# Performance work log

Measured on AMD Instinct MI355X. Metric: run time of the kernel, lower is better.

Reference implementation:

```python
import jax, jax.numpy as jnp
import numpy as np

N_NODES = 10000
N_EDGES = 320000
NODE_F = 64
EDGE_F = 32
H = 256
L = 6
HEADS = 8
OUT = H // HEADS
N_GRAPHS = 16
NEG_SLOPE = 0.2  # PyG GATConv leaky_relu slope


def setup_inputs() -> dict:
    key = jax.random.key(0)
    ks = jax.random.split(key, 32)
    s = 0.05
    f32 = jnp.float32
    inp = {}
    inp["x"] = jax.random.normal(ks[0], (N_NODES, NODE_F), f32)
    inp["edge_index"] = jax.random.randint(ks[1], (2, N_EDGES), 0, N_NODES)
    inp["edge_attr"] = jax.random.normal(ks[2], (N_EDGES, EDGE_F), f32)
    inp["batch"] = jnp.sort(jax.random.randint(ks[3], (N_NODES,), 0, N_GRAPHS))
    # embeddings
    inp["node_w"] = jax.random.normal(ks[4], (H, NODE_F), f32) * s
    inp["node_b"] = jnp.zeros((H,), f32)
    inp["edge_emb_w"] = jax.random.normal(ks[5], (H, EDGE_F), f32) * s
    inp["edge_emb_b"] = jnp.zeros((H,), f32)
    # stacked GATConv params (shared lin for src/dst since in_channels is int)
    inp["lin_w"] = jax.random.normal(ks[6], (L, H, H), f32) * s
    inp["att_src"] = jax.random.normal(ks[7], (L, HEADS, OUT), f32) * s
    inp["att_dst"] = jax.random.normal(ks[8], (L, HEADS, OUT), f32) * s
    inp["att_edge"] = jax.random.normal(ks[9], (L, HEADS, OUT), f32) * s
    inp["lin_edge_w"] = jax.random.normal(ks[10], (L, H, H), f32) * s
    inp["conv_b"] = jnp.zeros((L, H), f32)
    inp["ln_g"] = jnp.ones((L, H), f32)
    inp["ln_b"] = jnp.zeros((L, H), f32)
    # MLP heads: Linear(2H->H), Linear(H->H/2), Linear(H/2->3)
    inp["pw1"] = jax.random.normal(ks[11], (H, 2 * H), f32) * s
    inp["pb1"] = jnp.zeros((H,), f32)
    inp["pw2"] = jax.random.normal(ks[12], (H // 2, H), f32) * s
    inp["pb2"] = jnp.zeros((H // 2,), f32)
    inp["pw3"] = jax.random.normal(ks[13], (3, H // 2), f32) * s
    inp["pb3"] = jnp.zeros((3,), f32)
    inp["mw1"] = jax.random.normal(ks[14], (H, 2 * H), f32) * s
    inp["mb1"] = jnp.zeros((H,), f32)
    inp["mw2"] = jax.random.normal(ks[15], (H // 2, H), f32) * s
    inp["mb2"] = jnp.zeros((H // 2,), f32)
    inp["mw3"] = jax.random.normal(ks[16], (3, H // 2), f32) * s
    inp["mb3"] = jnp.zeros((3,), f32)
    return inp


def _ln(x, g, b):
    mu = jnp.mean(x, -1, keepdims=True)
    var = jnp.mean(jnp.square(x - mu), -1, keepdims=True)
    return g * (x - mu) * jax.lax.rsqrt(var + 1e-5) + b


def _mlp(z, w1, b1, w2, b2, w3, b3):
    h = jax.nn.gelu(z @ w1.T + b1, approximate=False)
    h = jax.nn.gelu(h @ w2.T + b2, approximate=False)
    return jax.nn.sigmoid(h @ w3.T + b3)


def _gnn_forward(x, edge_attr, src, dst, batch,
                 node_w, node_b, edge_emb_w, edge_emb_b,
                 lin_w, att_src, att_dst, att_edge, lin_edge_w, conv_b,
                 ln_g, ln_b,
                 pw1, pb1, pw2, pb2, pw3, pb3,
                 mw1, mb1, mw2, mb2, mw3, mb3):
    h = x @ node_w.T + node_b                       # [N, H]
    ea = edge_attr @ edge_emb_w.T + edge_emb_b      # [E, H]
    # PyG add_self_loops(fill_value='mean'): loop attr = mean of incoming edge attrs
    cnt = jax.ops.segment_sum(jnp.ones((N_EDGES,), h.dtype), dst, N_NODES)
    loop_attr = jax.ops.segment_sum(ea, dst, N_NODES) / jnp.maximum(cnt, 1.0)[:, None]
    ea_full = jnp.concatenate([ea, loop_attr], 0)   # [E+N, H]
    loops = jnp.arange(N_NODES, dtype=src.dtype)
    src_f = jnp.concatenate([src, loops])
    dst_f = jnp.concatenate([dst, loops])
    for i in range(L):
        x_in = h
        xw = (h @ lin_w[i].T).reshape(N_NODES, HEADS, OUT)
        eap = (ea_full @ lin_edge_w[i].T).reshape(-1, HEADS, OUT)
        a_src = jnp.sum(xw * att_src[i], -1)        # [N, heads]
        a_dst = jnp.sum(xw * att_dst[i], -1)
        alpha = a_src[src_f] + a_dst[dst_f] + jnp.sum(eap * att_edge[i], -1)  # [E+N, heads]
        alpha = jnp.where(alpha > 0, alpha, NEG_SLOPE * alpha)
        amax = jax.ops.segment_max(alpha, dst_f, N_NODES)
        e = jnp.exp(alpha - amax[dst_f])
        denom = jax.ops.segment_sum(e, dst_f, N_NODES)
        w = e / (denom[dst_f] + 1e-16)
        msg = xw[src_f] * w[:, :, None]             # [E+N, heads, out]
        hi = jax.ops.segment_sum(msg, dst_f, N_NODES).reshape(N_NODES, H) + conv_b[i]
        hi = jax.nn.gelu(_ln(hi, ln_g[i], ln_b[i]), approximate=False)
        h = hi + x_in if i > 0 else hi
    sums = jax.ops.segment_sum(h, batch, N_GRAPHS)  # [G, H]
    ncnt = jax.ops.segment_sum(jnp.ones((N_NODES,), h.dtype), batch, N_GRAPHS)
    mean = sums / jnp.maximum(ncnt, 1.0)[:, None]
    xg = jnp.concatenate([mean, sums], 1)           # [G, 2H]
    params = _mlp(xg, pw1, pb1, pw2, pb2, pw3, pb3)
    metrics = _mlp(xg, mw1, mb1, mw2, mb2, mw3, mb3)
    return params, metrics


def reference(x, edge_index, edge_attr, batch,
              node_w, node_b, edge_emb_w, edge_emb_b,
              lin_w, att_src, att_dst, att_edge, lin_edge_w, conv_b,
              ln_g, ln_b,
              pw1, pb1, pw2, pb2, pw3, pb3,
              mw1, mb1, mw2, mb2, mw3, mb3):
    return _gnn_forward(x, edge_attr, edge_index[0], edge_index[1], batch,
                        node_w, node_b, edge_emb_w, edge_emb_b,
                        lin_w, att_src, att_dst, att_edge, lin_edge_w, conv_b,
                        ln_g, ln_b,
                        pw1, pb1, pw2, pb2, pw3, pb3,
                        mw1, mb1, mw2, mb2, mw3, mb3)
```

## Files before the change

kernel.cpp:

```cpp
#include <hip/hip_runtime.h>
#include <math.h>

#define NN 10000
#define NE 320000
#define NODE_F 64
#define EDGE_F 32
#define HDIM 256
#define HEADS 8
#define LAYERS 6
#define NG 16
#define NPB 2
#define NOUT 48
#define LOG2E 1.4426950408889634f

typedef __attribute__((ext_vector_type(8))) short short8;
typedef __attribute__((ext_vector_type(4))) float float4v;
typedef __attribute__((ext_vector_type(2))) float floatx2;

__global__ void count_kernel(const int* __restrict__ dst, int* __restrict__ cnt) {
    int e = blockIdx.x * 256 + threadIdx.x;
    if (e < NE) atomicAdd(&cnt[dst[e]], 1);
}

__global__ void scan_kernel(const int* __restrict__ cnt, int* __restrict__ row_ptr,
                            int* __restrict__ pos) {
    __shared__ int wsum[16];
    __shared__ int woff[16];
    int t = threadIdx.x;
    int lane = t & 63, wid = t >> 6;
    const int chunk = 10;
    int lo = t * chunk;
    int loc[10];
    int s = 0;
    #pragma unroll
    for (int k = 0; k < 10; ++k) {
        int i = lo + k;
        int v = (i < NN) ? cnt[i] : 0;
        loc[k] = v;
        s += v;
    }
    int inc = s;
    #pragma unroll
    for (int off = 1; off < 64; off <<= 1) {
        int v = __shfl_up(inc, off, 64);
        if (lane >= off) inc += v;
    }
    if (lane == 63) wsum[wid] = inc;
    __syncthreads();
    if (t < 16) {
        int inc2 = wsum[t];
        #pragma unroll
        for (int off = 1; off < 16; off <<= 1) {
            int u = __shfl_up(inc2, off, 16);
            if (t >= off) inc2 += u;
        }
        woff[t] = inc2;
    }
    __syncthreads();
    int base = inc - s + (wid ? woff[wid - 1] : 0);
    #pragma unroll
    for (int k = 0; k < 10; ++k) {
        int i = lo + k;
        if (i < NN) {
            row_ptr[i] = base;
            pos[i] = base;
            base += loc[k];
        }
    }
    if (t == 1023) row_ptr[NN] = woff[15];
}

__global__ void scatter_kernel(const int* __restrict__ src, const int* __restrict__ dst,
                               int* __restrict__ pos, int2* __restrict__ csr_se) {
    int e = blockIdx.x * 256 + threadIdx.x;
    if (e >= NE) return;
    int d = dst[e];
    int idx = atomicAdd(&pos[d], 1);
    csr_se[idx] = make_int2(src[e], e);
}

__device__ __forceinline__ ushort f2bf(float f) {
    union { float f; unsigned u; } v; v.f = f;
    unsigned u = v.u;
    return (ushort)((u + 0x7fffu + ((u >> 16) & 1u)) >> 16);
}
__device__ __forceinline__ float bf2f(ushort b) {
    union { unsigned u; float f; } v; v.u = ((unsigned)b) << 16; return v.f;
}

__global__ __launch_bounds__(256) void prep_kernel(const float* __restrict__ att_edge,
                                                   const float* __restrict__ lin_edge_w,
                                                   const float* __restrict__ eew,
                                                   const float* __restrict__ eeb,
                                                   ushort* __restrict__ webbf,
                                                   float* __restrict__ bebuf) {
    int ih = blockIdx.x;
    int i = ih >> 3, h = ih & 7;
    __shared__ float vsh[HDIM];
    int t = threadIdx.x;
    float s = 0.f;
    const float* ae = att_edge + ih * 32;
    const float* lw = lin_edge_w + ((size_t)i * HDIM + h * 32) * HDIM + t;
    #pragma unroll
    for (int o = 0; o < 32; ++o) s += ae[o] * lw[(size_t)o * HDIM];
    vsh[t] = s;
    __syncthreads();
    if (t < EDGE_F) {
        float acc = 0.f;
        for (int k = 0; k < HDIM; ++k) acc += vsh[k] * eew[k * EDGE_F + t];
        webbf[ih * EDGE_F + t] = f2bf(acc * LOG2E);
    } else if (t == EDGE_F) {
        float acc = 0.f;
        for (int k = 0; k < HDIM; ++k) acc += vsh[k] * eeb[k];
        bebuf[ih] = acc * LOG2E;
    }
}

__global__ __launch_bounds__(64) void fold0_kernel(const float* __restrict__ lin_w,
                                                   const float* __restrict__ node_w,
                                                   const float* __restrict__ node_b,
                                                   ushort* __restrict__ w0p,
                                                   float* __restrict__ b0p) {
    int j = blockIdx.x, f = threadIdx.x;
    const float* wr = lin_w + (size_t)j * HDIM;
    float acc = 0.f, accb = 0.f;
    for (int k = 0; k < HDIM; ++k) acc += wr[k] * node_w[k * NODE_F + f];
    #pragma unroll
    for (int m = 0; m < 4; ++m) {
        int k = f + 64 * m;
        accb += wr[k] * node_b[k];
    }
    w0p[j * NODE_F + f] = f2bf(acc);
    #pragma unroll
    for (int off = 32; off >= 1; off >>= 1) accb += __shfl_xor(accb, off, 64);
    if (f == 0) b0p[j] = accb;
}

__global__ __launch_bounds__(256) void preE_kernel(const float* __restrict__ edge_attr,
                                                   const ushort* __restrict__ web,
                                                   const float* __restrict__ be,
                                                   ushort* __restrict__ preEb) {
    int wv = threadIdx.x >> 6, l = threadIdx.x & 63;
    int base = blockIdx.x * 64 + wv * 16;
    int m = l & 15, kq = (l >> 4) * 8;
    const float* ar = edge_attr + (size_t)(base + m) * EDGE_F + kq;
    float4 a0 = *(const float4*)(ar);
    float4 a1 = *(const float4*)(ar + 4);
    short8 afrag;
    afrag[0] = (short)f2bf(a0.x); afrag[1] = (short)f2bf(a0.y);
    afrag[2] = (short)f2bf(a0.z); afrag[3] = (short)f2bf(a0.w);
    afrag[4] = (short)f2bf(a1.x); afrag[5] = (short)f2bf(a1.y);
    afrag[6] = (short)f2bf(a1.z); afrag[7] = (short)f2bf(a1.w);
    float4v zero = {0.f, 0.f, 0.f, 0.f};
    float4v acc[3];
    #pragma unroll
    for (int ct = 0; ct < 3; ++ct) {
        short8 bfrag = *(const short8*)(web + (size_t)(ct * 16 + m) * EDGE_F + kq);
        acc[ct] = __builtin_amdgcn_mfma_f32_16x16x32_bf16(afrag, bfrag, zero, 0, 0, 0);
    }
    #pragma unroll
    for (int ct = 0; ct < 3; ++ct) {
        int oc = ct * 16 + m;
        int li = oc >> 3, hh = oc & 7;
        float bv = be[oc];
        #pragma unroll
        for (int r = 0; r < 4; ++r) {
            int row = (l >> 4) * 4 + r;
            preEb[(size_t)li * NE * 8 + (size_t)(base + row) * 8 + hh] = f2bf(acc[ct][r] + bv);
        }
    }
}

__global__ void tobf_all_kernel(const float* __restrict__ lin_w,
                                const float* __restrict__ x, ushort* __restrict__ wbhi,
                                ushort* __restrict__ xhi) {
    const int N1 = LAYERS * HDIM * HDIM;
    const int N2 = N1 + NN * NODE_F;
    int i = blockIdx.x * 256 + threadIdx.x;
    if (i < N1) wbhi[i] = f2bf(lin_w[i]);
    else if (i < N2) xhi[i - N1] = f2bf(x[i - N1]);
}

__global__ __launch_bounds__(128) void gemm_bf1(const ushort* __restrict__ Ah,
                                                const ushort* __restrict__ Bh,
                                                const float* __restrict__ bias,
                                                unsigned char* __restrict__ Cf8,
                                                const float* __restrict__ att_s,
                                                const float* __restrict__ att_d,
                                                float* __restrict__ a_src,
                                                float* __restrict__ a_dst,
                                                int N, int K) {
    __shared__ ushort sAh[64][40], sBh[64][40];
    int nb = blockIdx.y * 64, jb = blockIdx.x * 64;
    int t = threadIdx.x, w = t >> 6, l = t & 63;
    int srow = t >> 1, sq = (t & 1) * 16;
    int fr = l & 15, fq = (l >> 4) * 8;
    float4v acc[2][4] = {};
    for (int kt = 0; kt < K; kt += 32) {
        int gr = nb + srow;
        short8 a0 = {0,0,0,0,0,0,0,0}, a1 = {0,0,0,0,0,0,0,0};
        if (gr < N) {
            const short8* pa = (const short8*)(Ah + (size_t)gr * K + kt + sq);
            a0 = pa[0]; a1 = pa[1];
        }
        *(short8*)&sAh[srow][sq] = a0; *(short8*)&sAh[srow][sq + 8] = a1;
        const short8* pb = (const short8*)(Bh + (size_t)(jb + srow) * K + kt + sq);
        short8 b0 = pb[0], b1 = pb[1];
        *(short8*)&sBh[srow][sq] = b0; *(short8*)&sBh[srow][sq + 8] = b1;
        __syncthreads();
        short8 bh[4];
        #pragma unroll
        for (int nt = 0; nt < 4; ++nt)
            bh[nt] = *(const short8*)&sBh[nt * 16 + fr][fq];
        #pragma unroll
        for (int mt = 0; mt < 2; ++mt) {
            short8 ah = *(const short8*)&sAh[w * 32 + mt * 16 + fr][fq];
            #pragma unroll
            for (int nt = 0; nt < 4; ++nt)
                acc[mt][nt] = __builtin_amdgcn_mfma_f32_16x16x32_bf16(ah, bh[nt], acc[mt][nt], 0, 0, 0);
        }
        __syncthreads();
    }
    if (bias) {
        #pragma unroll
        for (int nt = 0; nt < 4; ++nt) {
            float bv = bias[jb + nt * 16 + fr];
            #pragma unroll
            for (int mt = 0; mt < 2; ++mt)
                #pragma unroll
                for (int r = 0; r < 4; ++r) acc[mt][nt][r] += bv;
        }
    }
    #pragma unroll
    for (int mt = 0; mt < 2; ++mt) {
        #pragma unroll
        for (int nt = 0; nt < 4; ++nt) {
            int col = jb + nt * 16 + fr;
            #pragma unroll
            for (int r = 0; r < 4; ++r) {
                int row = nb + w * 32 + mt * 16 + (l >> 4) * 4 + r;
                if (row < N) {
                    float v = acc[mt][nt][r];
                    int pk8 = __builtin_amdgcn_cvt_pk_fp8_f32(v, v, 0, false);
                    Cf8[(size_t)row * HDIM + col] = (unsigned char)(pk8 & 0xff);
                }
            }
        }
    }
    {
        int head0 = jb >> 5;
        float cs[4], cd[4];
        #pragma unroll
        for (int nt = 0; nt < 4; ++nt) {
            cs[nt] = att_s[jb + nt * 16 + fr] * LOG2E;
            cd[nt] = att_d[jb + nt * 16 + fr] * LOG2E;
        }
        #pragma unroll
        for (int mt = 0; mt < 2; ++mt) {
            #pragma unroll
            for (int r = 0; r < 4; ++r) {
                float s0 = acc[mt][0][r] * cs[0] + acc[mt][1][r] * cs[1];
                float s1 = acc[mt][2][r] * cs[2] + acc[mt][3][r] * cs[3];
                float d0 = acc[mt][0][r] * cd[0] + acc[mt][1][r] * cd[1];
                float d1 = acc[mt][2][r] * cd[2] + acc[mt][3][r] * cd[3];
                #pragma unroll
                for (int off = 8; off >= 1; off >>= 1) {
                    s0 += __shfl_xor(s0, off, 16);
                    s1 += __shfl_xor(s1, off, 16);
                    d0 += __shfl_xor(d0, off, 16);
                    d1 += __shfl_xor(d1, off, 16);
                }
                if (fr == 0) {
                    int row = nb + w * 32 + mt * 16 + (l >> 4) * 4 + r;
                    if (row < N) {
                        a_src[row * 8 + head0]     = s0;
                        a_src[row * 8 + head0 + 1] = s1;
                        a_dst[row * 8 + head0]     = d0;
                        a_dst[row * 8 + head0 + 1] = d1;
                    }
                }
            }
        }
    }
}

__device__ __forceinline__ float gelu_exact(float x) {
    return 0.5f * x * (1.f + erff(x * 0.70710678118654752f));
}

__global__ __launch_bounds__(64 * NPB) void node_kernel(const unsigned char* __restrict__ xwf8,
                                                  const ushort* __restrict__ pb,
                                                  const float* __restrict__ a_src,
                                                  const float* __restrict__ a_dst,
                                                  const int* __restrict__ row_ptr,
                                                  const int2* __restrict__ csr_se,
                                                  const ushort* __restrict__ hp,
                                                  ushort* __restrict__ hout,
                                                  const float* __restrict__ cb,
                                                  const float* __restrict__ lg,
                                                  const float* __restrict__ lb, int first) {
    int wv = threadIdx.x >> 6, l = threadIdx.x & 63;
    int n = blockIdx.x * NPB + wv;
    int start = row_ptr[n], end = row_ptr[n + 1];
    int hc = l >> 3;
    int hc8 = l & 56;
    int jj = l & 7;
    float adnh = a_dst[n * 8 + hc];
    const unsigned char* xb = xwf8 + 4 * l;

    float den = 0.f, acc[4] = {0.f, 0.f, 0.f, 0.f};
    float psum = 0.f;
    for (int idx = start; idx < end; idx += 8) {
        int myi = idx + jj;
        bool valid = myi < end;
        int2 se = valid ? csr_se[myi] : make_int2(n, 0);
        int snj[8];
        #pragma unroll
        for (int j = 0; j < 8; ++j) snj[j] = __shfl(se.x, hc8 + j, 64);
        unsigned g[8];
        #pragma unroll
        for (int j = 0; j < 8; ++j) g[j] = *(const unsigned*)(xb + (size_t)snj[j] * HDIM);
        float w_t = 0.f;
        if (valid) {
            float p_t = bf2f(pb[(size_t)se.y * 8 + hc]);
            float a_t = a_src[(size_t)se.x * 8 + hc] + adnh + p_t;
            w_t = exp2f(fminf(fmaxf(a_t, 0.2f * a_t), 57.7f));
            psum += p_t;
        }
        #pragma unroll
        for (int j = 0; j < 8; ++j) {
            float wj = __shfl(w_t, hc8 + j, 64);
            floatx2 lo = __builtin_amdgcn_cvt_pk_f32_fp8(g[j], false);
            floatx2 hi = __builtin_amdgcn_cvt_pk_f32_fp8(g[j], true);
            den += wj;
            acc[0] += wj * lo.x;
            acc[1] += wj * lo.y;
            acc[2] += wj * hi.x;
            acc[3] += wj * hi.y;
        }
    }
    #pragma unroll
    for (int off = 1; off < 8; off <<= 1) psum += __shfl_xor(psum, off, 64);
    int deg = end - start;
    float preLv = deg > 0 ? psum / (float)deg : 0.f;
    {
        float al = a_src[n * 8 + hc] + adnh + preLv;
        al = fminf(fmaxf(al, 0.2f * al), 57.7f);
        float wself = exp2f(al);
        den += wself;
        unsigned gs = *(const unsigned*)(xb + (size_t)n * HDIM);
        floatx2 lo = __builtin_amdgcn_cvt_pk_f32_fp8(gs, false);
        floatx2 hi = __builtin_amdgcn_cvt_pk_f32_fp8(gs, true);
        acc[0] += wself * lo.x;
        acc[1] += wself * lo.y;
        acc[2] += wself * hi.x;
        acc[3] += wself * hi.y;
    }
    float4 cb4 = *(const float4*)(cb + 4 * l);
    float invh = 1.f / (den + 1e-16f);
    acc[0] = acc[0] * invh + cb4.x;
    acc[1] = acc[1] * invh + cb4.y;
    acc[2] = acc[2] * invh + cb4.z;
    acc[3] = acc[3] * invh + cb4.w;

    float part = acc[0] + acc[1] + acc[2] + acc[3];
    #pragma unroll
    for (int off = 32; off >= 1; off >>= 1) part += __shfl_xor(part, off, 64);
    float mu = part * (1.f / 256.f);
    float p2 = 0.f;
    #pragma unroll
    for (int j = 0; j < 4; ++j) {
        float d = acc[j] - mu;
        p2 += d * d;
    }
    #pragma unroll
    for (int off = 32; off >= 1; off >>= 1) p2 += __shfl_xor(p2, off, 64);
    float rstd = rsqrtf(p2 * (1.f / 256.f) + 1e-5f);

    float4 lg4 = *(const float4*)(lg + 4 * l);
    float4 lb4 = *(const float4*)(lb + 4 * l);
    float o4[4];
    float lgv[4] = {lg4.x, lg4.y, lg4.z, lg4.w};
    float lbv[4] = {lb4.x, lb4.y, lb4.z, lb4.w};
    float hpv[4] = {0.f, 0.f, 0.f, 0.f};
    if (!first) {
        uint2 ph = *(const uint2*)(hp + (size_t)n * HDIM + 4 * l);
        hpv[0] = bf2f((ushort)(ph.x & 0xffff));
        hpv[1] = bf2f((ushort)(ph.x >> 16));
        hpv[2] = bf2f((ushort)(ph.y & 0xffff));
        hpv[3] = bf2f((ushort)(ph.y >> 16));
    }
    #pragma unroll
    for (int j = 0; j < 4; ++j) {
        float y = (acc[j] - mu) * rstd * lgv[j] + lbv[j];
        o4[j] = gelu_exact(y) + hpv[j];
    }
    uint2 po;
    po.x = (unsigned)f2bf(o4[0]) | ((unsigned)f2bf(o4[1]) << 16);
    po.y = (unsigned)f2bf(o4[2]) | ((unsigned)f2bf(o4[3]) << 16);
    *(uint2*)(hout + (size_t)n * HDIM + 4 * l) = po;
}

__global__ __launch_bounds__(256) void graph_sum_kernel(const ushort* __restrict__ h,
                                                        const int* __restrict__ batch,
                                                        float* __restrict__ sums) {
    int t = threadIdx.x;
    int n0 = blockIdx.x * 64;
    int n1 = min(NN, n0 + 64);
    float acc = 0.f;
    int cur = batch[n0];
    for (int n = n0; n < n1; ++n) {
        int b = batch[n];
        if (b != cur) {
            atomicAdd(&sums[cur * HDIM + t], acc);
            acc = 0.f;
            cur = b;
        }
        acc += bf2f(h[(size_t)n * HDIM + t]);
    }
    atomicAdd(&sums[cur * HDIM + t], acc);
}

__device__ __forceinline__ int lower_bound_dev(const int* a, int n, int v) {
    int lo = 0, hi = n;
    while (lo < hi) {
        int mid = (lo + hi) >> 1;
        if (a[mid] < v) lo = mid + 1; else hi = mid;
    }
    return lo;
}

__global__ __launch_bounds__(256) void mlp_kernel(const float* __restrict__ sums,
                                                  const int* __restrict__ batch,
                                                  const float* __restrict__ pw1,
                                                  const float* __restrict__ pb1,
                                                  const float* __restrict__ pw2,
                                                  const float* __restrict__ pb2,
                                                  const float* __restrict__ pw3,
                                                  const float* __restrict__ pb3,
                                                  const float* __restrict__ mw1,
                                                  const float* __restrict__ mb1,
                                                  const float* __restrict__ mw2,
                                                  const float* __restrict__ mb2,
                                                  const float* __restrict__ mw3,
                                                  const float* __restrict__ mb3,
                                                  float* __restrict__ out) {
    int g = blockIdx.x, which = blockIdx.y;
    const float* w1 = which ? mw1 : pw1; const float* b1 = which ? mb1 : pb1;
    const float* w2 = which ? mw2 : pw2; const float* b2 = which ? mb2 : pb2;
    const float* w3 = which ? mw3 : pw3; const float* b3 = which ? mb3 : pb3;
    __shared__ float xg[512];
    __shared__ float h1[256];
    __shared__ float h2[128];
    __shared__ float cinv_s;
    int t = threadIdx.x;
    if (t == 0) {
        int s0 = lower_bound_dev(batch, NN, g), s1 = lower_bound_dev(batch, NN, g + 1);
        cinv_s = 1.f / fmaxf((float)(s1 - s0), 1.f);
    }
    __syncthreads();
    float sv = sums[g * HDIM + t];
    xg[t] = sv * cinv_s;
    xg[256 + t] = sv;
    __syncthreads();
    {
        const float* wr = w1 + (size_t)t * 512;
        float acc = 0.f;
        #pragma unroll 8
        for (int k = 0; k < 512; k += 4) {
            float4 wv = *(const float4*)(wr + k);
            acc += wv.x * xg[k] + wv.y * xg[k + 1] + wv.z * xg[k + 2] + wv.w * xg[k + 3];
        }
        h1[t] = gelu_exact(acc + b1[t]);
    }
    __syncthreads();
    {
        int row = t >> 1, hf = t & 1;
        const float* wr = w2 + (size_t)row * 256 + hf * 128;
        const float* hx = h1 + hf * 128;
        float acc = 0.f;
        #pragma unroll 8
        for (int k = 0; k < 128; k += 4) {
            float4 wv = *(const float4*)(wr + k);
            acc += wv.x * hx[k] + wv.y * hx[k + 1] + wv.z * hx[k + 2] + wv.w * hx[k + 3];
        }
        acc += __shfl_xor(acc, 1, 64);
        if (hf == 0) h2[row] = gelu_exact(acc + b2[row]);
    }
    __syncthreads();
    if (t < 64) {
        float v0 = h2[t], v1 = h2[64 + t];
        #pragma unroll
        for (int o = 0; o < 3; ++o) {
            float p = w3[o * 128 + t] * v0 + w3[o * 128 + 64 + t] * v1;
            #pragma unroll
            for (int off = 32; off >= 1; off >>= 1) p += __shfl_xor(p, off, 64);
            if (t == 0) out[which * (NG * 3) + g * 3 + o] = 1.f / (1.f + expf(-(p + b3[o])));
        }
    }
}

extern "C" void kernel_launch(void* const* d_in, const int* in_sizes, int n_in, void* d_out,
                              int out_size, void* d_ws, size_t ws_size, hipStream_t stream) {
    const float* x         = (const float*)d_in[0];
    const int*   ei        = (const int*)d_in[1];
    const int*   src       = ei;
    const int*   dst       = ei + NE;
    const float* edge_attr = (const float*)d_in[2];
    const int*   batch     = (const int*)d_in[3];
    const float* node_w    = (const float*)d_in[4];
    const float* node_b    = (const float*)d_in[5];
    const float* eew       = (const float*)d_in[6];
    const float* eeb       = (const float*)d_in[7];
    const float* lin_w     = (const float*)d_in[8];
    const float* att_src   = (const float*)d_in[9];
    const float* att_dst   = (const float*)d_in[10];
    const float* att_edge  = (const float*)d_in[11];
    const float* lin_edge_w= (const float*)d_in[12];
    const float* conv_b    = (const float*)d_in[13];
    const float* ln_g      = (const float*)d_in[14];
    const float* ln_b      = (const float*)d_in[15];
    const float* pw1 = (const float*)d_in[16]; const float* pb1 = (const float*)d_in[17];
    const float* pw2 = (const float*)d_in[18]; const float* pb2 = (const float*)d_in[19];
    const float* pw3 = (const float*)d_in[20]; const float* pb3 = (const float*)d_in[21];
    const float* mw1 = (const float*)d_in[22]; const float* mb1 = (const float*)d_in[23];
    const float* mw2 = (const float*)d_in[24]; const float* mb2 = (const float*)d_in[25];
    const float* mw3 = (const float*)d_in[26]; const float* mb3 = (const float*)d_in[27];
    float* out = (float*)d_out;

    float* wsf = (float*)d_ws;
    float* a_src     = wsf; wsf += (size_t)NN * HEADS;
    float* a_dst     = wsf; wsf += (size_t)NN * HEADS;
    float* bebuf     = wsf; wsf += 64;
    float* b0p       = wsf; wsf += HDIM;
    ushort* ubuf = (ushort*)wsf;
    ushort* preEb = ubuf; ubuf += (size_t)NE * NOUT;
    ushort* webbf = ubuf; ubuf += (size_t)NOUT * EDGE_F;
    ushort* hb0  = ubuf; ubuf += (size_t)NN * HDIM;
    ushort* hb1  = ubuf; ubuf += (size_t)NN * HDIM;
    unsigned char* xwf8 = (unsigned char*)ubuf; ubuf += (size_t)NN * HDIM / 2;
    ushort* wbhi = ubuf; ubuf += (size_t)LAYERS * HDIM * HDIM;
    ushort* xhi  = ubuf; ubuf += (size_t)NN * NODE_F;
    ushort* w0p  = ubuf; ubuf += (size_t)HDIM * NODE_F;
    int* ibuf    = (int*)ubuf;
    int* cnt     = ibuf; ibuf += NN + 16;
    float* sums  = (float*)ibuf; ibuf += NG * HDIM;
    int* row_ptr = ibuf; ibuf += NN + 16;
    int* pos     = ibuf; ibuf += NN + 16;
    int2* csr_se = (int2*)ibuf; ibuf += 2 * NE;

    hipMemsetAsync(cnt, 0, (NN + 16 + NG * HDIM) * sizeof(int), stream);
    count_kernel<<<(NE + 255) / 256, 256, 0, stream>>>(dst, cnt);
    scan_kernel<<<1, 1024, 0, stream>>>(cnt, row_ptr, pos);
    scatter_kernel<<<(NE + 255) / 256, 256, 0, stream>>>(src, dst, pos, csr_se);

    prep_kernel<<<LAYERS * HEADS, 256, 0, stream>>>(att_edge, lin_edge_w, eew, eeb, webbf, bebuf);
    preE_kernel<<<NE / 64, 256, 0, stream>>>(edge_attr, webbf, bebuf, preEb);

    {
        const int total = LAYERS * HDIM * HDIM + NN * NODE_F;
        tobf_all_kernel<<<(total + 255) / 256, 256, 0, stream>>>(lin_w, x, wbhi, xhi);
    }
    fold0_kernel<<<HDIM, 64, 0, stream>>>(lin_w, node_w, node_b, w0p, b0p);

    ushort* hb[2] = {hb0, hb1};
    for (int i = 0; i < LAYERS; ++i) {
        dim3 grid(HDIM / 64, (NN + 63) / 64);
        const ushort* Ain = (i == 0) ? xhi : hb[(i - 1) & 1];
        const ushort* Bin = (i == 0) ? w0p : wbhi + (size_t)i * HDIM * HDIM;
        int Kin = (i == 0) ? NODE_F : HDIM;
        const float* bias = (i == 0) ? b0p : nullptr;
        gemm_bf1<<<grid, 128, 0, stream>>>(Ain, Bin, bias, xwf8,
                                           att_src + i * HEADS * 32, att_dst + i * HEADS * 32,
                                           a_src, a_dst, NN, Kin);
        node_kernel<<<NN / NPB, 64 * NPB, 0, stream>>>(
            xwf8, preEb + (size_t)i * NE * 8, a_src, a_dst,
            row_ptr, csr_se, (i == 0) ? nullptr : hb[(i - 1) & 1], hb[i & 1],
            conv_b + i * HDIM, ln_g + i * HDIM, ln_b + i * HDIM, i == 0 ? 1 : 0);
    }

    graph_sum_kernel<<<(NN + 63) / 64, 256, 0, stream>>>(hb[(LAYERS - 1) & 1], batch, sums);
    {
        dim3 gm(NG, 2);
        mlp_kernel<<<gm, 256, 0, stream>>>(sums, batch, pw1, pb1, pw2, pb2, pw3, pb3,
                                           mw1, mb1, mw2, mb2, mw3, mb3, out);
    }
}
```

Baseline: 477.3 us.

## Split node aggregation across two waves per node and fuse degree count into preE

The node kernel now assigns one node per 128-thread block. The two waves take alternating 8-edge chunks of the neighbor list and combine their partial sums through shared memory before the layernorm/GELU epilogue. This is meant to halve the serial gather latency per node and raise memory-level parallelism, at the cost of a sync, LDS traffic and duplicated epilogue math. The separate degree-counting kernel is also folded into preE_kernel, which removes one launch.

```diff
diff --git a/kernel.cpp b/kernel.cpp
--- a/kernel.cpp
+++ b/kernel.cpp
@@ -9,18 +9,12 @@
 #define HEADS 8
 #define LAYERS 6
 #define NG 16
-#define NPB 2
 #define NOUT 48
 #define LOG2E 1.4426950408889634f
 
 typedef __attribute__((ext_vector_type(8))) short short8;
 typedef __attribute__((ext_vector_type(4))) float float4v;
 typedef __attribute__((ext_vector_type(2))) float floatx2;
-
-__global__ void count_kernel(const int* __restrict__ dst, int* __restrict__ cnt) {
-    int e = blockIdx.x * 256 + threadIdx.x;
-    if (e < NE) atomicAdd(&cnt[dst[e]], 1);
-}
 
 __global__ void scan_kernel(const int* __restrict__ cnt, int* __restrict__ row_ptr,
                             int* __restrict__ pos) {
@@ -139,8 +133,12 @@
 __global__ __launch_bounds__(256) void preE_kernel(const float* __restrict__ edge_attr,
                                                    const ushort* __restrict__ web,
                                                    const float* __restrict__ be,
-                                                   ushort* __restrict__ preEb) {
-    int wv = threadIdx.x >> 6, l = threadIdx.x & 63;
+                                                   ushort* __restrict__ preEb,
+                                                   const int* __restrict__ dst,
+                                                   int* __restrict__ cnt) {
+    int t = threadIdx.x;
+    if (t < 64) atomicAdd(&cnt[dst[blockIdx.x * 64 + t]], 1);
+    int wv = t >> 6, l = t & 63;
     int base = blockIdx.x * 64 + wv * 16;
     int m = l & 15, kq = (l >> 4) * 8;
     const float* ar = edge_attr + (size_t)(base + m) * EDGE_F + kq;
@@ -288,7 +286,7 @@
     return 0.5f * x * (1.f + erff(x * 0.70710678118654752f));
 }
 
-__global__ __launch_bounds__(64 * NPB) void node_kernel(const unsigned char* __restrict__ xwf8,
+__global__ __launch_bounds__(128) void node_kernel(const unsigned char* __restrict__ xwf8,
                                                   const ushort* __restrict__ pb,
                                                   const float* __restrict__ a_src,
                                                   const float* __restrict__ a_dst,
@@ -299,8 +297,10 @@
                                                   const float* __restrict__ cb,
                                                   const float* __restrict__ lg,
                                                   const float* __restrict__ lb, int first) {
-    int wv = threadIdx.x >> 6, l = threadIdx.x & 63;
-    int n = blockIdx.x * NPB + wv;
+    __shared__ float red[6][128];
+    int t = threadIdx.x;
+    int wv = t >> 6, l = t & 63;
+    int n = blockIdx.x;
     int start = row_ptr[n], end = row_ptr[n + 1];
     int hc = l >> 3;
     int hc8 = l & 56;
@@ -310,7 +310,7 @@
 
     float den = 0.f, acc[4] = {0.f, 0.f, 0.f, 0.f};
     float psum = 0.f;
-    for (int idx = start; idx < end; idx += 8) {
+    for (int idx = start + wv * 8; idx < end; idx += 16) {
         int myi = idx + jj;
         bool valid = myi < end;
         int2 se = valid ? csr_se[myi] : make_int2(n, 0);
@@ -341,6 +341,13 @@
     }
     #pragma unroll
     for (int off = 1; off < 8; off <<= 1) psum += __shfl_xor(psum, off, 64);
+    red[0][t] = den; red[1][t] = acc[0]; red[2][t] = acc[1];
+    red[3][t] = acc[2]; red[4][t] = acc[3]; red[5][t] = psum;
+    __syncthreads();
+    int ot = t ^ 64;
+    den += red[0][ot]; acc[0] += red[1][ot]; acc[1] += red[2][ot];
+    acc[2] += red[3][ot]; acc[3] += red[4][ot]; psum += red[5][ot];
+
     int deg = end - start;
     float preLv = deg > 0 ? psum / (float)deg : 0.f;
     {
@@ -377,28 +384,30 @@
     for (int off = 32; off >= 1; off >>= 1) p2 += __shfl_xor(p2, off, 64);
     float rstd = rsqrtf(p2 * (1.f / 256.f) + 1e-5f);
 
-    float4 lg4 = *(const float4*)(lg + 4 * l);
-    float4 lb4 = *(const float4*)(lb + 4 * l);
-    float o4[4];
-    float lgv[4] = {lg4.x, lg4.y, lg4.z, lg4.w};
-    float lbv[4] = {lb4.x, lb4.y, lb4.z, lb4.w};
-    float hpv[4] = {0.f, 0.f, 0.f, 0.f};
-    if (!first) {
-        uint2 ph = *(const uint2*)(hp + (size_t)n * HDIM + 4 * l);
-        hpv[0] = bf2f((ushort)(ph.x & 0xffff));
-        hpv[1] = bf2f((ushort)(ph.x >> 16));
-        hpv[2] = bf2f((ushort)(ph.y & 0xffff));
-        hpv[3] = bf2f((ushort)(ph.y >> 16));
-    }
-    #pragma unroll
-    for (int j = 0; j < 4; ++j) {
-        float y = (acc[j] - mu) * rstd * lgv[j] + lbv[j];
-        o4[j] = gelu_exact(y) + hpv[j];
-    }
-    uint2 po;
-    po.x = (unsigned)f2bf(o4[0]) | ((unsigned)f2bf(o4[1]) << 16);
-    po.y = (unsigned)f2bf(o4[2]) | ((unsigned)f2bf(o4[3]) << 16);
-    *(uint2*)(hout + (size_t)n * HDIM + 4 * l) = po;
+    if (wv == 0) {
+        float4 lg4 = *(const float4*)(lg + 4 * l);
+        float4 lb4 = *(const float4*)(lb + 4 * l);
+        float o4[4];
+        float lgv[4] = {lg4.x, lg4.y, lg4.z, lg4.w};
+        float lbv[4] = {lb4.x, lb4.y, lb4.z, lb4.w};
+        float hpv[4] = {0.f, 0.f, 0.f, 0.f};
+        if (!first) {
+            uint2 ph = *(const uint2*)(hp + (size_t)n * HDIM + 4 * l);
+            hpv[0] = bf2f((ushort)(ph.x & 0xffff));
+            hpv[1] = bf2f((ushort)(ph.x >> 16));
+            hpv[2] = bf2f((ushort)(ph.y & 0xffff));
+            hpv[3] = bf2f((ushort)(ph.y >> 16));
+        }
+        #pragma unroll
+        for (int j = 0; j < 4; ++j) {
+            float y = (acc[j] - mu) * rstd * lgv[j] + lbv[j];
+            o4[j] = gelu_exact(y) + hpv[j];
+        }
+        uint2 po;
+        po.x = (unsigned)f2bf(o4[0]) | ((unsigned)f2bf(o4[1]) << 16);
+        po.y = (unsigned)f2bf(o4[2]) | ((unsigned)f2bf(o4[3]) << 16);
+        *(uint2*)(hout + (size_t)n * HDIM + 4 * l) = po;
+    }
 }
 
 __global__ __launch_bounds__(256) void graph_sum_kernel(const ushort* __restrict__ h,
@@ -550,12 +559,12 @@
     int2* csr_se = (int2*)ibuf; ibuf += 2 * NE;
 
     hipMemsetAsync(cnt, 0, (NN + 16 + NG * HDIM) * sizeof(int), stream);
-    count_kernel<<<(NE + 255) / 256, 256, 0, stream>>>(dst, cnt);
+
+    prep_kernel<<<LAYERS * HEADS, 256, 0, stream>>>(att_edge, lin_edge_w, eew, eeb, webbf, bebuf);
+    preE_kernel<<<NE / 64, 256, 0, stream>>>(edge_attr, webbf, bebuf, preEb, dst, cnt);
+
     scan_kernel<<<1, 1024, 0, stream>>>(cnt, row_ptr, pos);
     scatter_kernel<<<(NE + 255) / 256, 256, 0, stream>>>(src, dst, pos, csr_se);
-
-    prep_kernel<<<LAYERS * HEADS, 256, 0, stream>>>(att_edge, lin_edge_w, eew, eeb, webbf, bebuf);
-    preE_kernel<<<NE / 64, 256, 0, stream>>>(edge_attr, webbf, bebuf, preEb);
 
     {
         const int total = LAYERS * HDIM * HDIM + NN * NODE_F;
@@ -573,7 +582,7 @@
         gemm_bf1<<<grid, 128, 0, stream>>>(Ain, Bin, bias, xwf8,
                                            att_src + i * HEADS * 32, att_dst + i * HEADS * 32,
                                            a_src, a_dst, NN, Kin);
-        node_kernel<<<NN / NPB, 64 * NPB, 0, stream>>>(
+        node_kernel<<<NN, 128, 0, stream>>>(
             xwf8, preEb + (size_t)i * NE * 8, a_src, a_dst,
             row_ptr, csr_se, (i == 0) ? nullptr : hb[(i - 1) & 1], hb[i & 1],
             conv_b + i * HDIM, ln_g + i * HDIM, ln_b + i * HDIM, i == 0 ? 1 : 0);
```

Result: no change. 473.0 us (-0.9%).
